# Kernel optimization log

Measured on AMD Instinct MI355X. Metric: run time of the kernel, lower is better.

Reference implementation:

```python
import jax, jax.numpy as jnp
import numpy as np
from jax import lax

H_SIZE = 2048
NUM_K = 16
NUM_V = 32
DK = 128
DV = 128
KDIM = NUM_K * DK      # 2048
VDIM = NUM_V * DV      # 4096
KCONV = 4
RMS_EPS = 1e-6
L2_EPS = 1e-6


def l2norm(x, eps=L2_EPS):
    # matches torch l2norm: x * rsqrt(sum(x^2, -1) + eps)
    return x * lax.rsqrt(jnp.sum(x * x, axis=-1, keepdims=True) + eps)


def setup_inputs() -> dict:
    key = jax.random.key(0)
    ks = jax.random.split(key, 7)
    B, S = 2, 1024
    conv_dim = 2 * KDIM + VDIM  # 8192
    return {
        "hidden_states": jax.random.normal(ks[0], (B, S, H_SIZE), jnp.float32),
        "w_qkvz": jax.random.normal(ks[1], (H_SIZE, 2 * KDIM + 2 * VDIM), jnp.float32) * 0.02,
        "w_ba": jax.random.normal(ks[2], (H_SIZE, 2 * NUM_V), jnp.float32) * 0.02,
        "conv_w": jax.random.normal(ks[3], (conv_dim, 1, KCONV), jnp.float32) * 0.2,  # depthwise [C,1,K]
        "dt_bias": jnp.ones((NUM_V,), jnp.float32),
        "A_log": jnp.log(jax.random.uniform(ks[4], (NUM_V,), jnp.float32, 0.5, 8.0)),
        "norm_w": jnp.ones((DV,), jnp.float32),
        "w_out": jax.random.normal(ks[5], (VDIM, H_SIZE), jnp.float32) * 0.02,
    }


def _forward(hidden_states, w_qkvz, w_ba, conv_w, dt_bias, A_log, norm_w, w_out):
    B, S, _ = hidden_states.shape
    rf = NUM_V // NUM_K  # GQA repeat factor = 2

    # input projections
    qkvz = hidden_states @ w_qkvz                                  # [B,S,12288]
    ba = hidden_states @ w_ba                                      # [B,S,64]

    # fix_query_key_value_ordering: group per k-head then split
    qkvz = qkvz.reshape(B, S, NUM_K, 2 * DK + 2 * rf * DV)
    q, k, v, z = jnp.split(qkvz, [DK, 2 * DK, 2 * DK + rf * DV], axis=3)
    ba = ba.reshape(B, S, NUM_K, 2 * rf)
    b, a = jnp.split(ba, [rf], axis=3)
    v = v.reshape(B, S, NUM_V, DV)
    z = z.reshape(B, S, NUM_V, DV)
    b = b.reshape(B, S, NUM_V)
    a = a.reshape(B, S, NUM_V)

    # depthwise causal conv over [q|k|v] channels + silu
    mixed = jnp.concatenate(
        [q.reshape(B, S, KDIM), k.reshape(B, S, KDIM), v.reshape(B, S, VDIM)], axis=-1
    )                                                              # [B,S,conv_dim]
    x = mixed.transpose(0, 2, 1)                                   # [B,C,S]
    x = jnp.pad(x, ((0, 0), (0, 0), (KCONV - 1, 0)))
    x = lax.conv_general_dilated(x, conv_w, window_strides=(1,), padding="VALID",
                                 feature_group_count=x.shape[1])
    x = jax.nn.silu(x).transpose(0, 2, 1)                          # [B,S,conv_dim]

    q, k, v = jnp.split(x, [KDIM, 2 * KDIM], axis=-1)
    q = q.reshape(B, S, NUM_K, DK)
    k = k.reshape(B, S, NUM_K, DK)
    v = v.reshape(B, S, NUM_V, DV)

    beta = jax.nn.sigmoid(b)                                       # [B,S,NUM_V]
    g = -jnp.exp(A_log) * jax.nn.softplus(a + dt_bias)             # log-decay [B,S,NUM_V]

    if rf > 1:
        q = jnp.repeat(q, rf, axis=2)                              # [B,S,NUM_V,DK]
        k = jnp.repeat(k, rf, axis=2)
    q = l2norm(q) * (DK ** -0.5)
    k = l2norm(k)

    # gated delta rule recurrence over time via lax.scan
    S0 = jnp.zeros((B, NUM_V, DK, DV), q.dtype)

    def step(state, inp):
        q_t, k_t, v_t, g_t, b_t = inp                              # [B,H,dk]/[B,H,dv]/[B,H]
        state = state * jnp.exp(g_t)[..., None, None]              # decay
        kv_mem = jnp.einsum("bhkv,bhk->bhv", state, k_t)
        delta = (v_t - kv_mem) * b_t[..., None]
        state = state + jnp.einsum("bhk,bhv->bhkv", k_t, delta)
        o = jnp.einsum("bhkv,bhk->bhv", state, q_t)
        return state, o

    xs = (jnp.moveaxis(q, 1, 0), jnp.moveaxis(k, 1, 0), jnp.moveaxis(v, 1, 0),
          jnp.moveaxis(g, 1, 0), jnp.moveaxis(beta, 1, 0))
    _, out = lax.scan(step, S0, xs)
    out = jnp.moveaxis(out, 0, 1)                                  # [B,S,NUM_V,DV]

    # gated RMSNorm (gate applied before normalization, Mamba2 style)
    xg = out * jax.nn.silu(z)
    y = xg * lax.rsqrt(jnp.mean(xg * xg, axis=-1, keepdims=True) + RMS_EPS) * norm_w
    y = y.reshape(B, S, VDIM)
    return y @ w_out                                               # [B,S,H_SIZE]


def reference(hidden_states, w_qkvz, w_ba, conv_w, dt_bias, A_log, norm_w, w_out):
    return _forward(hidden_states, w_qkvz, w_ba, conv_w, dt_bias, A_log, norm_w, w_out)
```

## Files before the change

kernel.cpp:

```cpp
#include <hip/hip_runtime.h>
#include <stdint.h>

#define AS1 __attribute__((address_space(1)))
#define AS3 __attribute__((address_space(3)))

typedef __bf16 bf16x8 __attribute__((ext_vector_type(8)));
typedef float f32x4 __attribute__((ext_vector_type(4)));

static __device__ __forceinline__ float bf2f(unsigned short u) {
    union { unsigned int i; float f; } x; x.i = ((unsigned int)u) << 16; return x.f;
}
static __device__ __forceinline__ unsigned short f2bf(float f) {
    union { float f; unsigned int i; } x; x.f = f;
    unsigned int u = x.i;
    unsigned int r = (u + 0x7fffu + ((u >> 16) & 1u)) >> 16;
    return (unsigned short)r;
}

static __device__ __forceinline__ void gll16(const void* g, void* l) {
    __builtin_amdgcn_global_load_lds((const AS1 unsigned int*)g,
                                     (AS3 unsigned int*)l, 16, 0, 0);
}

__global__ __launch_bounds__(256) void cvt_bf16_kernel(
    const float* __restrict__ src, unsigned short* __restrict__ dst, int n4) {
    int i = blockIdx.x * 256 + threadIdx.x;
    if (i >= n4) return;
    float4 v = ((const float4*)src)[i];
    ushort4 o;
    o.x = f2bf(v.x); o.y = f2bf(v.y); o.z = f2bf(v.z); o.w = f2bf(v.w);
    ((ushort4*)dst)[i] = o;
}

__global__ __launch_bounds__(256) void transpose_cvt_kernel(
    const float* __restrict__ src, unsigned short* __restrict__ dst, int R, int C) {
    __shared__ float tile[32][33];
    int x = threadIdx.x & 31, y = threadIdx.x >> 5;
    int c0 = blockIdx.x * 32, r0 = blockIdx.y * 32;
#pragma unroll
    for (int i = 0; i < 4; i++)
        tile[y + i * 8][x] = src[(size_t)(r0 + y + i * 8) * C + (c0 + x)];
    __syncthreads();
#pragma unroll
    for (int i = 0; i < 4; i++)
        dst[(size_t)(c0 + y + i * 8) * R + (r0 + x)] = f2bf(tile[x][y + i * 8]);
}

template <int MODE>
__global__ __launch_bounds__(512, 2) void gemm256_kernel(
    const unsigned short* __restrict__ A, const unsigned short* __restrict__ Bt,
    void* __restrict__ C, int M, int N, int K, int Ksl) {
    __shared__ __align__(16) unsigned short SH[65536];
    int tid = threadIdx.x;
    int lane = tid & 63, w = tid >> 6;
    int wr = w >> 2, wc = w & 3;
    int qd = lane >> 4, rc = lane & 15;

    int m0, n0, zz = 0;
    if (MODE == 0) {
        int wg = blockIdx.x;
        int xcd = wg & 7, loc = wg >> 3;
        m0 = (loc / 6) * 256;
        n0 = (xcd * 6 + loc % 6) * 256;
    } else {
        int wg = blockIdx.x;
        zz = wg >> 6;
        int loc = wg & 63;
        m0 = (loc >> 3) * 256;
        n0 = (loc & 7) * 256;
    }
    const int NT = Ksl >> 6;
    const int sK = K << 7;

    size_t sr[2];
#pragma unroll
    for (int j = 0; j < 2; j++) {
        int bu = j * 4096 + tid * 8;
        int sub = bu >> 9;
        int b = bu & 511;
        int bp = b ^ (((b >> 8) & 1) << 4);
        int row = ((sub >> 1) << 4) + (bp >> 5);
        int col = ((sub & 1) << 5) + (bp & 31);
        sr[j] = (size_t)row * K + col;
    }
    const unsigned short* Ab = A + (size_t)m0 * K + (size_t)zz * Ksl;
    const unsigned short* Bb = Bt + (size_t)n0 * K + (size_t)zz * Ksl;

    const int foff = (rc * 32 + qd * 8) ^ (((rc >> 3) & 1) << 4);
    const int Ah = wr;
    const int Bh = wc >> 1;
    const int brow4 = (wc & 1) * 4;

    f32x4 acc[8][4];
#pragma unroll
    for (int i = 0; i < 8; i++)
#pragma unroll
        for (int j = 0; j < 4; j++)
#pragma unroll
            for (int r = 0; r < 4; r++) acc[i][j][r] = 0.f;

    bf16x8 aq[4][2], bq[4][2];

#define STG(mat, h, t)                                                        \
    {                                                                         \
        const unsigned short* s_ = ((mat) ? Bb : Ab) + (h) * sK + (t) * 64;   \
        int d_ = ((mat) << 15) + (((((t) & 1) * 2 + (h))) << 13) + tid * 8;   \
        gll16(s_ + sr[0], &SH[d_]);                                           \
        gll16(s_ + sr[1], &SH[d_ + 4096]);                                    \
    }

#define LDAQ(p, QR)                                                           \
    {                                                                         \
        int ab_ = ((p) * 2 + Ah) * 8192 + (QR) * 4096 + foff;                 \
        _Pragma("unroll") for (int fi = 0; fi < 4; fi++)                      \
            _Pragma("unroll") for (int ks = 0; ks < 2; ks++)                  \
                aq[fi][ks] = *(const bf16x8*)&SH[ab_ + (fi * 2 + ks) * 512];  \
    }

#define LDBQ(p)                                                               \
    {                                                                         \
        int bb_ = 32768 + ((p) * 2 + Bh) * 8192 + brow4 * 1024 + foff;        \
        _Pragma("unroll") for (int fg = 0; fg < 4; fg++)                      \
            _Pragma("unroll") for (int ks = 0; ks < 2; ks++)                  \
                bq[fg][ks] = *(const bf16x8*)&SH[bb_ + (fg * 2 + ks) * 512];  \
    }

#define MFMAQ(QR, QC)                                                         \
    {                                                                         \
        _Pragma("unroll") for (int fi = 0; fi < 4; fi++)                      \
            _Pragma("unroll") for (int fj = 0; fj < 2; fj++)                  \
                _Pragma("unroll") for (int ks = 0; ks < 2; ks++)              \
                    acc[(QR) * 4 + fi][(QC) * 2 + fj] =                       \
                        __builtin_amdgcn_mfma_f32_16x16x32_bf16(              \
                            aq[fi][ks], bq[(QC) * 2 + fj][ks],                \
                            acc[(QR) * 4 + fi][(QC) * 2 + fj], 0, 0, 0);      \
    }

#define FENCE asm volatile("" ::: "memory")
#define BARRIER { FENCE; __builtin_amdgcn_s_barrier(); FENCE; }
#define LGKM0 asm volatile("s_waitcnt lgkmcnt(0)" ::: "memory")

    STG(0, 0, 0); STG(0, 1, 0); STG(1, 0, 0); STG(1, 1, 0);
    STG(1, 0, 1); STG(1, 1, 1); STG(0, 0, 1);
    asm volatile("s_waitcnt vmcnt(6)" ::: "memory");
    BARRIER;

    for (int g = 0; g < NT; ++g) {
        const int p = g & 1;
        LDAQ(p, 0);
        LDBQ(p);
        if (g + 1 < NT) STG(0, 1, g + 1);
        BARRIER; LGKM0;
        __builtin_amdgcn_s_setprio(1);
        MFMAQ(0, 0);
        __builtin_amdgcn_s_setprio(0);
        BARRIER;
        if (g + 2 < NT) STG(1, 0, g + 2);
        BARRIER; LGKM0;
        __builtin_amdgcn_s_setprio(1);
        MFMAQ(0, 1);
        __builtin_amdgcn_s_setprio(0);
        BARRIER;
        LDAQ(p, 1);
        if (g + 2 < NT) STG(1, 1, g + 2);
        BARRIER; LGKM0;
        __builtin_amdgcn_s_setprio(1);
        MFMAQ(1, 0);
        __builtin_amdgcn_s_setprio(0);
        BARRIER;
        if (g + 2 < NT) STG(0, 0, g + 2);
        if (g < NT - 2) { asm volatile("s_waitcnt vmcnt(6)" ::: "memory"); }
        else            { asm volatile("s_waitcnt vmcnt(0)" ::: "memory"); }
        BARRIER; LGKM0;
        __builtin_amdgcn_s_setprio(1);
        MFMAQ(1, 1);
        __builtin_amdgcn_s_setprio(0);
        BARRIER;
    }

#undef STG
#undef LDAQ
#undef LDBQ
#undef MFMAQ
#undef FENCE
#undef BARRIER
#undef LGKM0

    if (MODE == 0) {
        unsigned short* Cp = (unsigned short*)C;
#pragma unroll
        for (int mi = 0; mi < 8; mi++) {
            int row = m0 + wr * 128 + mi * 16 + qd * 4;
#pragma unroll
            for (int fg = 0; fg < 4; fg++) {
                int col = n0 + wc * 64 + fg * 16 + rc;
#pragma unroll
                for (int r = 0; r < 4; r++)
                    Cp[(size_t)(row + r) * N + col] = f2bf(acc[mi][fg][r]);
            }
        }
    } else {
        float* Cf = (float*)C + (size_t)zz * M * N;
#pragma unroll
        for (int mi = 0; mi < 8; mi++) {
            int row = m0 + wr * 128 + mi * 16 + qd * 4;
#pragma unroll
            for (int fg = 0; fg < 4; fg++) {
                int col = n0 + wc * 64 + fg * 16 + rc;
#pragma unroll
                for (int r = 0; r < 4; r++)
                    Cf[(size_t)(row + r) * N + col] = acc[mi][fg][r];
            }
        }
    }
}

__global__ __launch_bounds__(256) void add_out4_kernel(
    const float* __restrict__ p, float* __restrict__ out, int n4) {
    int i = blockIdx.x * 256 + threadIdx.x;
    if (i >= n4) return;
    size_t st = (size_t)n4 * 4;
    float4 a = ((const float4*)p)[i];
    float4 b = ((const float4*)(p + st))[i];
    float4 c = ((const float4*)(p + 2 * st))[i];
    float4 d = ((const float4*)(p + 3 * st))[i];
    ((float4*)out)[i] = make_float4(a.x + b.x + c.x + d.x, a.y + b.y + c.y + d.y,
                                    a.z + b.z + c.z + d.z, a.w + b.w + c.w + d.w);
}

__global__ __launch_bounds__(256) void bag_kernel(
    const float* __restrict__ hs, const float* __restrict__ w_ba,
    const float* __restrict__ A_log, const float* __restrict__ dt_bias,
    float* __restrict__ gg, float* __restrict__ bb) {
    int w = threadIdx.x >> 6, lane = threadIdx.x & 63;
    int r0 = blockIdx.x * 8 + w * 2;
    const float* h0 = hs + (size_t)r0 * 2048;
    float a0 = 0.f, a1 = 0.f;
    for (int k = 0; k < 2048; k++) {
        float wv = w_ba[k * 64 + lane];
        a0 += h0[k] * wv;
        a1 += h0[2048 + k] * wv;
    }
    int h = lane >> 2, idx = lane & 3;
    int vh = h * 2 + (idx & 1);
    float accs[2] = {a0, a1};
#pragma unroll
    for (int j = 0; j < 2; j++) {
        int t = r0 + j;
        float acc = accs[j];
        if (idx < 2) {
            bb[t * 32 + vh] = 1.f / (1.f + expf(-acc));
        } else {
            float x = acc + dt_bias[vh];
            float sp = fmaxf(x, 0.f) + log1pf(expf(-fabsf(x)));
            gg[t * 32 + vh] = -expf(A_log[vh]) * sp;
        }
    }
}

__global__ __launch_bounds__(256) void conv_kernel(
    const unsigned short* __restrict__ qkvz, const float* __restrict__ conv_w,
    unsigned short* __restrict__ qb, unsigned short* __restrict__ kb,
    float* __restrict__ vv) {
    __shared__ float xs[8192];
    __shared__ float rs[32];
    int t = blockIdx.x;
    int s = t & 1023;
    int tid = threadIdx.x;
    size_t rowbase = (size_t)t * 12288;
#pragma unroll
    for (int i = 0; i < 4; i++) {
        int c = (i * 256 + tid) * 8;
        int d = c & 127;
        int col;
        if (c < 2048) col = (c >> 7) * 768 + d;
        else if (c < 4096) col = ((c - 2048) >> 7) * 768 + 128 + d;
        else { int vh2 = (c - 4096) >> 7; col = (vh2 >> 1) * 768 + 256 + (vh2 & 1) * 128 + d; }
        float wts[8][4];
#pragma unroll
        for (int e = 0; e < 8; e++) {
            float4 t4 = *(const float4*)(conv_w + (size_t)(c + e) * 4);
            wts[e][0] = t4.x; wts[e][1] = t4.y; wts[e][2] = t4.z; wts[e][3] = t4.w;
        }
        float acc[8] = {0.f, 0.f, 0.f, 0.f, 0.f, 0.f, 0.f, 0.f};
#pragma unroll
        for (int j = 0; j < 4; j++) {
            int ss = s - 3 + j;
            if (ss >= 0) {
                uint4 u = *(const uint4*)(qkvz + rowbase + (size_t)(j - 3) * 12288 + col);
                const unsigned short* us = (const unsigned short*)&u;
#pragma unroll
                for (int e = 0; e < 8; e++) acc[e] += bf2f(us[e]) * wts[e][j];
            }
        }
#pragma unroll
        for (int e = 0; e < 8; e++) xs[c + e] = acc[e] / (1.f + expf(-acc[e]));
    }
    __syncthreads();
    {
        int seg = tid >> 3, part = tid & 7;
        const float* pp = xs + seg * 128 + part * 16;
        float s2 = 0.f;
#pragma unroll
        for (int j = 0; j < 16; j++) s2 += pp[j] * pp[j];
        s2 += __shfl_xor(s2, 1);
        s2 += __shfl_xor(s2, 2);
        s2 += __shfl_xor(s2, 4);
        if (part == 0) rs[seg] = rsqrtf(s2 + 1e-6f);
    }
    __syncthreads();
    const float QS = 0.08838834764831845f;
#pragma unroll
    for (int i = 0; i < 4; i++) {
        int c = (i * 256 + tid) * 8;
        float x[8];
#pragma unroll
        for (int e = 0; e < 8; e++) x[e] = xs[c + e];
        if (c < 4096) {
            float sc = (c < 2048) ? rs[c >> 7] * QS : rs[((c - 2048) >> 7) + 16];
            uint4 o;
            o.x = (unsigned)f2bf(x[0] * sc) | ((unsigned)f2bf(x[1] * sc) << 16);
            o.y = (unsigned)f2bf(x[2] * sc) | ((unsigned)f2bf(x[3] * sc) << 16);
            o.z = (unsigned)f2bf(x[4] * sc) | ((unsigned)f2bf(x[5] * sc) << 16);
            o.w = (unsigned)f2bf(x[6] * sc) | ((unsigned)f2bf(x[7] * sc) << 16);
            if (c < 2048) *(uint4*)(qb + (size_t)t * 2048 + c) = o;
            else *(uint4*)(kb + (size_t)t * 2048 + c - 2048) = o;
        } else {
            float* vp = vv + (size_t)t * 4096 + c - 4096;
            *(float4*)vp = make_float4(x[0], x[1], x[2], x[3]);
            *(float4*)(vp + 4) = make_float4(x[4], x[5], x[6], x[7]);
        }
    }
}

__global__ __launch_bounds__(256, 2) void prep_kernel(
    const unsigned short* __restrict__ qb, const unsigned short* __restrict__ kb,
    const float* __restrict__ vv, const float* __restrict__ gg,
    const float* __restrict__ bb,
    unsigned short* __restrict__ Wg, unsigned short* __restrict__ DlT,
    unsigned short* __restrict__ KtT, unsigned short* __restrict__ Pt,
    float* __restrict__ lamg, float* __restrict__ l64g) {
    __shared__ __align__(16) unsigned short Tb[64 * 72];
    __shared__ __align__(16) unsigned short Xw[4][64 * 72];
    __shared__ float Td[4 * 16 * 17];
    __shared__ float RHSw[4][16 * 68];
    __shared__ float cc[64], bet[64], lam_s[64], ex64[64];

    int bid = blockIdx.x;
    int ch = bid & 15, bh = bid >> 4;
    int vh = bh & 31, b = bh >> 5;
    int hk = vh >> 1;
    int t0 = b * 1024 + ch * 64;
    int tid = threadIdx.x, wv = tid >> 6, lane = tid & 63;
    int qd = lane >> 4, rc = lane & 15;
    int rowb = (wv & 1) * 32;
    size_t obase = (size_t)bid * 8192;
    size_t pbase = (size_t)bid * 4096;

    if (tid < 64) {
        float x = gg[(size_t)(t0 + tid) * 32 + vh];
#pragma unroll
        for (int ofs = 1; ofs < 64; ofs <<= 1) {
            float up = __shfl_up(x, ofs, 64);
            if (tid >= ofs) x += up;
        }
        cc[tid] = x;
        float l = __expf(x);
        lam_s[tid] = l;
        float tot = __shfl(x, 63, 64);
        ex64[tid] = __expf(tot - x);
        bet[tid] = bb[(size_t)(t0 + tid) * 32 + vh];
        lamg[(size_t)bid * 64 + tid] = l;
        if (tid == 0) l64g[bid] = __expf(tot);
    }
    __syncthreads();

    {
        const unsigned short* src = (wv >= 2) ? qb : kb;
        f32x4 acc[2][4];
#pragma unroll
        for (int tm = 0; tm < 2; tm++)
#pragma unroll
            for (int tn = 0; tn < 4; tn++)
#pragma unroll
                for (int r = 0; r < 4; r++) acc[tm][tn][r] = 0.f;
#pragma unroll
        for (int ks = 0; ks < 4; ks++) {
            bf16x8 af[2], bfr[4];
#pragma unroll
            for (int tm = 0; tm < 2; tm++) {
                int row = rowb + tm * 16 + rc;
                af[tm] = *(const bf16x8*)(src + ((size_t)(t0 + row) * 16 + hk) * 128 + ks * 32 + qd * 8);
            }
#pragma unroll
            for (int tn = 0; tn < 4; tn++)
                bfr[tn] = *(const bf16x8*)(kb + ((size_t)(t0 + tn * 16 + rc) * 16 + hk) * 128 + ks * 32 + qd * 8);
#pragma unroll
            for (int tm = 0; tm < 2; tm++)
#pragma unroll
                for (int tn = 0; tn < 4; tn++)
                    acc[tm][tn] = __builtin_amdgcn_mfma_f32_16x16x32_bf16(af[tm], bfr[tn], acc[tm][tn], 0, 0, 0);
        }
        if (wv < 2) {
#pragma unroll
            for (int tm = 0; tm < 2; tm++)
#pragma unroll
                for (int tn = 0; tn < 4; tn++)
#pragma unroll
                    for (int r = 0; r < 4; r++) {
                        int i = rowb + tm * 16 + qd * 4 + r;
                        int j = tn * 16 + rc;
                        float val = acc[tm][tn][r];
                        float tv = 0.f;
                        if (i > j) tv = bet[i] * __expf(cc[i] - cc[j]) * val;
                        Tb[i * 72 + j] = f2bf(-tv);
                        if ((i >> 4) == (j >> 4) && i > j)
                            Td[(i >> 4) * 272 + (i & 15) * 17 + (j & 15)] = tv;
                    }
        } else {
#pragma unroll
            for (int tm = 0; tm < 2; tm++)
#pragma unroll
                for (int tn = 0; tn < 4; tn++)
#pragma unroll
                    for (int r = 0; r < 4; r++) {
                        int i = rowb + tm * 16 + qd * 4 + r;
                        int j = tn * 16 + rc;
                        float ev = (i >= j) ? __expf(cc[i] - cc[j]) : 0.f;
                        Pt[pbase + i * 64 + j] = f2bf(ev * acc[tm][tn][r]);
                    }
        }
    }
    {
        int dk = tid >> 1, half = tid & 1;
#pragma unroll
        for (int j = 0; j < 4; j++) {
            unsigned short tmp[8];
#pragma unroll
            for (int e = 0; e < 8; e++) {
                int tok = half * 32 + j * 8 + e;
                tmp[e] = f2bf(bf2f(kb[((size_t)(t0 + tok) * 16 + hk) * 128 + dk]) * ex64[tok]);
            }
            *(uint4*)(KtT + obase + dk * 64 + half * 32 + j * 8) = *(const uint4*)tmp;
        }
    }
    __syncthreads();

    {
        int cb = wv;
        unsigned short* Xb = Xw[wv];
        float* RHS = RHSw[wv];
        for (int z = lane; z < 64 * 72 / 2; z += 64) ((unsigned int*)Xb)[z] = 0u;
#pragma unroll
        for (int B = 0; B < 4; B++) {
            f32x4 tacc[4];
#pragma unroll
            for (int cf = 0; cf < 4; cf++)
#pragma unroll
                for (int r = 0; r < 4; r++) {
                    int i = B * 16 + qd * 4 + r;
                    int c = cf * 16 + rc;
                    float v;
                    if (cb < 2)
                        v = bet[i] * vv[((size_t)(t0 + i) * 32 + vh) * 128 + cb * 64 + c];
                    else
                        v = bet[i] * lam_s[i] * bf2f(kb[((size_t)(t0 + i) * 16 + hk) * 128 + (cb - 2) * 64 + c]);
                    tacc[cf][r] = v;
                }
            __builtin_amdgcn_s_waitcnt(0xc07f);
            const int nks = (B + 1) >> 1;
#pragma unroll
            for (int ks = 0; ks < 2; ks++) {
                if (ks >= nks) break;
                bf16x8 af = *(const bf16x8*)&Tb[(B * 16 + rc) * 72 + ks * 32 + qd * 8];
#pragma unroll
                for (int cf = 0; cf < 4; cf++) {
                    bf16x8 bf_ = *(const bf16x8*)&Xb[(cf * 16 + rc) * 72 + ks * 32 + qd * 8];
                    tacc[cf] = __builtin_amdgcn_mfma_f32_16x16x32_bf16(af, bf_, tacc[cf], 0, 0, 0);
                }
            }
#pragma unroll
            for (int cf = 0; cf < 4; cf++)
#pragma unroll
                for (int r = 0; r < 4; r++)
                    RHS[(qd * 4 + r) * 68 + cf * 16 + rc] = tacc[cf][r];
            __builtin_amdgcn_s_waitcnt(0xc07f);
            {
                float d[16];
#pragma unroll
                for (int i2 = 0; i2 < 16; i2++) d[i2] = RHS[i2 * 68 + lane];
#pragma unroll
                for (int i2 = 1; i2 < 16; i2++)
#pragma unroll
                    for (int j2 = 0; j2 < i2; j2++)
                        d[i2] -= Td[B * 272 + i2 * 17 + j2] * d[j2];
#pragma unroll
                for (int i2 = 0; i2 < 16; i2++)
                    Xb[lane * 72 + B * 16 + i2] = f2bf(d[i2]);
            }
        }
        __builtin_amdgcn_s_waitcnt(0xc07f);
        if (cb < 2) {
#pragma unroll
            for (int j = 0; j < 8; j++) {
                uint4 u = *(const uint4*)&Xb[lane * 72 + j * 8];
                *(uint4*)(DlT + obase + (size_t)(cb * 64 + lane) * 64 + j * 8) = u;
            }
        } else {
#pragma unroll
            for (int dq = 0; dq < 8; dq++) {
                unsigned short tmp[8];
#pragma unroll
                for (int e = 0; e < 8; e++)
                    tmp[e] = Xb[(dq * 8 + e) * 72 + lane];
                *(uint4*)(Wg + obase + (size_t)lane * 128 + (cb - 2) * 64 + dq * 8) = *(const uint4*)tmp;
            }
        }
    }
}

__global__ __launch_bounds__(256, 2) void recb_kernel(
    const unsigned short* __restrict__ qb, const float* __restrict__ lamg,
    const float* __restrict__ l64g, const unsigned short* __restrict__ Wg,
    const unsigned short* __restrict__ DlT, const unsigned short* __restrict__ KtT,
    const unsigned short* __restrict__ Pt, float* __restrict__ oo) {
    __shared__ __align__(16) unsigned short St[16 * 136];
    __shared__ __align__(16) unsigned short Dls[16 * 72];
    int bid = blockIdx.x;
    int slice = bid >> 6;
    int rest = bid & 63;
    int vh = rest & 31, b = rest >> 5;
    int bh = b * 32 + vh;
    int hk = vh >> 1, dvo = slice * 16, tb = b * 1024;
    int tid = threadIdx.x, wv = tid >> 6, lane = tid & 63;
    int qd = lane >> 4, rc = lane & 15;

    f32x4 sacc[2];
#pragma unroll
    for (int tm = 0; tm < 2; tm++)
#pragma unroll
        for (int r = 0; r < 4; r++) sacc[tm][r] = 0.f;
    for (int z = tid; z < 16 * 136 / 2; z += 256) ((unsigned int*)St)[z] = 0u;
    __syncthreads();

#pragma unroll 1
    for (int ch = 0; ch < 16; ch++) {
        int bhch = bh * 16 + ch;
        size_t obase = (size_t)bhch * 8192;
        size_t pbase = (size_t)bhch * 4096;
        int t0 = tb + ch * 64;
        if (tid < 128) {
            int row = tid >> 3, t8 = (tid & 7) * 8;
            uint4 u = *(const uint4*)(DlT + obase + (dvo + row) * 64 + t8);
            *(uint4*)&Dls[row * 72 + t8] = u;
        }
        __syncthreads();
        {
            f32x4 uacc;
#pragma unroll
            for (int r = 0; r < 4; r++) uacc[r] = 0.f;
#pragma unroll
            for (int ks = 0; ks < 4; ks++) {
                bf16x8 a_ = *(const bf16x8*)&St[rc * 136 + ks * 32 + qd * 8];
                bf16x8 b_ = *(const bf16x8*)(Wg + obase + (size_t)(wv * 16 + rc) * 128 + ks * 32 + qd * 8);
                uacc = __builtin_amdgcn_mfma_f32_16x16x32_bf16(a_, b_, uacc, 0, 0, 0);
            }
#pragma unroll
            for (int r = 0; r < 4; r++) {
                int idx = (qd * 4 + r) * 72 + wv * 16 + rc;
                Dls[idx] = f2bf(bf2f(Dls[idx]) - uacc[r]);
            }
        }
        __syncthreads();
        {
            f32x4 qacc;
#pragma unroll
            for (int r = 0; r < 4; r++) qacc[r] = 0.f;
#pragma unroll
            for (int ks = 0; ks < 4; ks++) {
                bf16x8 a_ = *(const bf16x8*)(qb + ((size_t)(t0 + wv * 16 + rc) * 16 + hk) * 128 + ks * 32 + qd * 8);
                bf16x8 b_ = *(const bf16x8*)&St[rc * 136 + ks * 32 + qd * 8];
                qacc = __builtin_amdgcn_mfma_f32_16x16x32_bf16(a_, b_, qacc, 0, 0, 0);
            }
            bf16x8 bd[2];
#pragma unroll
            for (int ks = 0; ks < 2; ks++)
                bd[ks] = *(const bf16x8*)&Dls[rc * 72 + ks * 32 + qd * 8];
            f32x4 oacc;
#pragma unroll
            for (int r = 0; r < 4; r++)
                oacc[r] = lamg[(size_t)bhch * 64 + wv * 16 + qd * 4 + r] * qacc[r];
#pragma unroll
            for (int ks = 0; ks < 2; ks++) {
                bf16x8 a_ = *(const bf16x8*)(Pt + pbase + (size_t)(wv * 16 + rc) * 64 + ks * 32 + qd * 8);
                oacc = __builtin_amdgcn_mfma_f32_16x16x32_bf16(a_, bd[ks], oacc, 0, 0, 0);
            }
#pragma unroll
            for (int r = 0; r < 4; r++)
                oo[((size_t)(t0 + wv * 16 + qd * 4 + r) * 32 + vh) * 128 + dvo + rc] = oacc[r];
            float l64 = l64g[bhch];
#pragma unroll
            for (int tm = 0; tm < 2; tm++) {
#pragma unroll
                for (int r = 0; r < 4; r++) sacc[tm][r] *= l64;
#pragma unroll
                for (int ks = 0; ks < 2; ks++) {
                    bf16x8 a_ = *(const bf16x8*)(KtT + obase + (size_t)(wv * 32 + tm * 16 + rc) * 64 + ks * 32 + qd * 8);
                    sacc[tm] = __builtin_amdgcn_mfma_f32_16x16x32_bf16(a_, bd[ks], sacc[tm], 0, 0, 0);
                }
            }
        }
        __syncthreads();
#pragma unroll
        for (int tm = 0; tm < 2; tm++)
#pragma unroll
            for (int r = 0; r < 4; r++)
                St[rc * 136 + wv * 32 + tm * 16 + qd * 4 + r] = f2bf(sacc[tm][r]);
        __syncthreads();
    }
}

__global__ __launch_bounds__(256) void norm_kernel(
    const float* __restrict__ oo, const unsigned short* __restrict__ qkvz,
    const float* __restrict__ norm_w, unsigned short* __restrict__ yb) {
    int w = threadIdx.x >> 6, lane = threadIdx.x & 63;
    int g = blockIdx.x * 4 + w;
    int t = g >> 5, vh = g & 31;
    size_t ob = (size_t)g * 128;
    size_t zb = (size_t)t * 12288 + (size_t)(vh >> 1) * 768 + 512 + (vh & 1) * 128;
    float x0 = oo[ob + lane], x1 = oo[ob + 64 + lane];
    float z0 = bf2f(qkvz[zb + lane]), z1 = bf2f(qkvz[zb + 64 + lane]);
    float xg0 = x0 * (z0 / (1.f + expf(-z0)));
    float xg1 = x1 * (z1 / (1.f + expf(-z1)));
    float s = xg0 * xg0 + xg1 * xg1;
    s += __shfl_xor(s, 1);
    s += __shfl_xor(s, 2);
    s += __shfl_xor(s, 4);
    s += __shfl_xor(s, 8);
    s += __shfl_xor(s, 16);
    s += __shfl_xor(s, 32);
    float r = rsqrtf(s * (1.f / 128.f) + 1e-6f);
    size_t y0 = (size_t)t * 4096 + (size_t)vh * 128;
    yb[y0 + lane] = f2bf(xg0 * r * norm_w[lane]);
    yb[y0 + 64 + lane] = f2bf(xg1 * r * norm_w[64 + lane]);
}

extern "C" void kernel_launch(void* const* d_in, const int* in_sizes, int n_in,
                              void* d_out, int out_size, void* d_ws, size_t ws_size,
                              hipStream_t stream) {
    const float* hs      = (const float*)d_in[0];
    const float* w_qkvz  = (const float*)d_in[1];
    const float* w_ba    = (const float*)d_in[2];
    const float* conv_w  = (const float*)d_in[3];
    const float* dt_bias = (const float*)d_in[4];
    const float* A_log   = (const float*)d_in[5];
    const float* norm_w  = (const float*)d_in[6];
    const float* w_out   = (const float*)d_in[7];
    float* out = (float*)d_out;
    (void)in_sizes; (void)n_in; (void)out_size; (void)ws_size;

    char* p = (char*)d_ws;
    auto alloc = [&](size_t b) { char* r = p; p += (b + 255) & ~(size_t)255; return r; };
    float* gg = (float*)alloc(2048ull * 32 * 4);
    float* bb = (float*)alloc(2048ull * 32 * 4);
    unsigned short* hsb  = (unsigned short*)alloc(2048ull * 2048 * 2);
    unsigned short* woT  = (unsigned short*)alloc(2048ull * 4096 * 2);
    unsigned short* wqT  = (unsigned short*)alloc(12288ull * 2048 * 2);
    unsigned short* qkvz = (unsigned short*)alloc(2048ull * 12288 * 2);
    unsigned short* qb16 = (unsigned short*)alloc(2048ull * 2048 * 2);
    unsigned short* kb16 = (unsigned short*)alloc(2048ull * 2048 * 2);
    float* vv = (float*)alloc(2048ull * 4096 * 4);
    float* oo = (float*)alloc(2048ull * 4096 * 4);
    unsigned short* yb = (unsigned short*)alloc(2048ull * 4096 * 2);
    unsigned short* Wg  = (unsigned short*)alloc(1024ull * 8192 * 2);
    unsigned short* DlT = (unsigned short*)alloc(1024ull * 8192 * 2);
    unsigned short* KtT = (unsigned short*)alloc(1024ull * 8192 * 2);
    unsigned short* Pt  = (unsigned short*)alloc(1024ull * 4096 * 2);
    float* lamg = (float*)alloc(1024ull * 64 * 4);
    float* l64g = (float*)alloc(1024ull * 4);
    float* gpart = (float*)wqT;

    cvt_bf16_kernel<<<4096, 256, 0, stream>>>(hs, hsb, 2048 * 2048 / 4);
    transpose_cvt_kernel<<<dim3(12288 / 32, 2048 / 32), 256, 0, stream>>>(w_qkvz, wqT, 2048, 12288);
    transpose_cvt_kernel<<<dim3(2048 / 32, 4096 / 32), 256, 0, stream>>>(w_out, woT, 4096, 2048);
    gemm256_kernel<0><<<384, 512, 0, stream>>>(hsb, wqT, qkvz, 2048, 12288, 2048, 2048);
    bag_kernel<<<256, 256, 0, stream>>>(hs, w_ba, A_log, dt_bias, gg, bb);
    conv_kernel<<<2048, 256, 0, stream>>>(qkvz, conv_w, qb16, kb16, vv);
    prep_kernel<<<1024, 256, 0, stream>>>(qb16, kb16, vv, gg, bb, Wg, DlT, KtT, Pt, lamg, l64g);
    recb_kernel<<<512, 256, 0, stream>>>(qb16, lamg, l64g, Wg, DlT, KtT, Pt, oo);
    norm_kernel<<<16384, 256, 0, stream>>>(oo, qkvz, norm_w, yb);
    gemm256_kernel<1><<<256, 512, 0, stream>>>(yb, woT, gpart, 2048, 2048, 4096, 1024);
    add_out4_kernel<<<4096, 256, 0, stream>>>(gpart, out, 2048 * 2048 / 4);
}
```

Baseline: 733.5 us.

## Use 128x384 tiles for QKVZ projection GEMM and remap conv block order

Adds a dedicated GEMM kernel for the input projection that uses 128x384 output tiles, giving 512 workgroups instead of 384 so they divide evenly across the GPU's compute units and XCDs. The old MODE template is split into this kernel plus a float-output split-K kernel for the output projection. The conv kernel's block index is also remapped so blocks are interleaved across XCDs. The aim is better load balance with no tail wave, at the cost of a smaller M tile with less A reuse and a different LDS layout for B.

```diff
diff --git a/kernel.cpp b/kernel.cpp
--- a/kernel.cpp
+++ b/kernel.cpp
@@ -46,29 +46,164 @@
         dst[(size_t)(c0 + y + i * 8) * R + (r0 + x)] = f2bf(tile[x][y + i * 8]);
 }
 
-template <int MODE>
-__global__ __launch_bounds__(512, 2) void gemm256_kernel(
+#define FENCE asm volatile("" ::: "memory")
+#define BARRIER { FENCE; __builtin_amdgcn_s_barrier(); FENCE; }
+#define LGKM0 asm volatile("s_waitcnt lgkmcnt(0)" ::: "memory")
+
+__global__ __launch_bounds__(512, 2) void gemm384_kernel(
     const unsigned short* __restrict__ A, const unsigned short* __restrict__ Bt,
-    void* __restrict__ C, int M, int N, int K, int Ksl) {
+    unsigned short* __restrict__ C, int M, int N, int K) {
     __shared__ __align__(16) unsigned short SH[65536];
     int tid = threadIdx.x;
     int lane = tid & 63, w = tid >> 6;
     int wr = w >> 2, wc = w & 3;
     int qd = lane >> 4, rc = lane & 15;
 
-    int m0, n0, zz = 0;
-    if (MODE == 0) {
-        int wg = blockIdx.x;
-        int xcd = wg & 7, loc = wg >> 3;
-        m0 = (loc / 6) * 256;
-        n0 = (xcd * 6 + loc % 6) * 256;
-    } else {
-        int wg = blockIdx.x;
-        zz = wg >> 6;
-        int loc = wg & 63;
-        m0 = (loc >> 3) * 256;
-        n0 = (loc & 7) * 256;
-    }
+    int wg = blockIdx.x;
+    int xcd = wg & 7, loc = wg >> 3;
+    int m0 = (loc & 15) * 128;
+    int n0 = (xcd * 4 + (loc >> 4)) * 384;
+
+    const int NT = K >> 6;
+    const int sK = K << 7;
+
+    size_t sr[2];
+#pragma unroll
+    for (int j = 0; j < 2; j++) {
+        int bu = j * 4096 + tid * 8;
+        int sub = bu >> 9;
+        int b = bu & 511;
+        int bp = b ^ (((b >> 8) & 1) << 4);
+        int row = ((sub >> 1) << 4) + (bp >> 5);
+        int col = ((sub & 1) << 5) + (bp & 31);
+        sr[j] = (size_t)row * K + col;
+    }
+    const unsigned short* Ab = A + (size_t)m0 * K;
+    const unsigned short* Bb = Bt + (size_t)n0 * K;
+
+    const int foff = (rc * 32 + qd * 8) ^ (((rc >> 3) & 1) << 4);
+    int bC[6];
+#pragma unroll
+    for (int fj = 0; fj < 6; fj++) {
+        int nb = wc * 96 + fj * 16;
+        bC[fj] = (1 + (nb >> 7)) * 16384 + ((nb & 127) >> 4) * 1024 + foff;
+    }
+
+    f32x4 acc[4][6];
+#pragma unroll
+    for (int i = 0; i < 4; i++)
+#pragma unroll
+        for (int j = 0; j < 6; j++)
+#pragma unroll
+            for (int r = 0; r < 4; r++) acc[i][j][r] = 0.f;
+
+    bf16x8 aq[2][2], bq[6][2];
+
+#define STG(u, t)                                                             \
+    {                                                                         \
+        const unsigned short* s_ =                                            \
+            ((u) == 0 ? Ab : Bb + (size_t)((u)-1) * sK) + (size_t)(t) * 64;   \
+        int d_ = (((u)*2 + ((t)&1)) << 13) + tid * 8;                         \
+        gll16(s_ + sr[0], &SH[d_]);                                           \
+        gll16(s_ + sr[1], &SH[d_ + 4096]);                                    \
+    }
+
+#define LDAQ(p, QR)                                                           \
+    {                                                                         \
+        _Pragma("unroll") for (int fi = 0; fi < 2; fi++)                      \
+            _Pragma("unroll") for (int ks = 0; ks < 2; ks++)                  \
+                aq[fi][ks] = *(const bf16x8*)&SH[(p)*8192 +                   \
+                    (wr * 4 + (QR)*2 + fi) * 1024 + ks * 512 + foff];         \
+    }
+
+#define LDBQ(p)                                                               \
+    {                                                                         \
+        _Pragma("unroll") for (int fj = 0; fj < 6; fj++)                      \
+            _Pragma("unroll") for (int ks = 0; ks < 2; ks++)                  \
+                bq[fj][ks] = *(const bf16x8*)&SH[bC[fj] + (p)*8192 + ks*512]; \
+    }
+
+#define MFMAQ(QR, QC)                                                         \
+    {                                                                         \
+        _Pragma("unroll") for (int fi = 0; fi < 2; fi++)                      \
+            _Pragma("unroll") for (int fj = 0; fj < 3; fj++)                  \
+                _Pragma("unroll") for (int ks = 0; ks < 2; ks++)              \
+                    acc[(QR)*2 + fi][(QC)*3 + fj] =                           \
+                        __builtin_amdgcn_mfma_f32_16x16x32_bf16(              \
+                            aq[fi][ks], bq[(QC)*3 + fj][ks],                  \
+                            acc[(QR)*2 + fi][(QC)*3 + fj], 0, 0, 0);          \
+    }
+
+    STG(0, 0); STG(1, 0); STG(2, 0); STG(3, 0);
+    STG(1, 1); STG(2, 1); STG(3, 1);
+    asm volatile("s_waitcnt vmcnt(6)" ::: "memory");
+    BARRIER;
+
+    for (int g = 0; g < NT; ++g) {
+        const int p = g & 1;
+        LDAQ(p, 0);
+        LDBQ(p);
+        if (g + 1 < NT) STG(0, g + 1);
+        BARRIER; LGKM0;
+        __builtin_amdgcn_s_setprio(1);
+        MFMAQ(0, 0);
+        __builtin_amdgcn_s_setprio(0);
+        BARRIER;
+        if (g + 2 < NT) STG(1, g + 2);
+        BARRIER; LGKM0;
+        __builtin_amdgcn_s_setprio(1);
+        MFMAQ(0, 1);
+        __builtin_amdgcn_s_setprio(0);
+        BARRIER;
+        LDAQ(p, 1);
+        if (g + 2 < NT) STG(2, g + 2);
+        BARRIER; LGKM0;
+        __builtin_amdgcn_s_setprio(1);
+        MFMAQ(1, 0);
+        __builtin_amdgcn_s_setprio(0);
+        BARRIER;
+        if (g + 2 < NT) STG(3, g + 2);
+        if (g < NT - 2) { asm volatile("s_waitcnt vmcnt(6)" ::: "memory"); }
+        else            { asm volatile("s_waitcnt vmcnt(0)" ::: "memory"); }
+        BARRIER; LGKM0;
+        __builtin_amdgcn_s_setprio(1);
+        MFMAQ(1, 1);
+        __builtin_amdgcn_s_setprio(0);
+        BARRIER;
+    }
+
+#undef STG
+#undef LDAQ
+#undef LDBQ
+#undef MFMAQ
+
+#pragma unroll
+    for (int mi = 0; mi < 4; mi++) {
+        int row = m0 + wr * 64 + mi * 16 + qd * 4;
+#pragma unroll
+        for (int fj = 0; fj < 6; fj++) {
+            int col = n0 + wc * 96 + fj * 16 + rc;
+#pragma unroll
+            for (int r = 0; r < 4; r++)
+                C[(size_t)(row + r) * N + col] = f2bf(acc[mi][fj][r]);
+        }
+    }
+}
+
+__global__ __launch_bounds__(512, 2) void gemm256_kernel(
+    const unsigned short* __restrict__ A, const unsigned short* __restrict__ Bt,
+    float* __restrict__ C, int M, int N, int K, int Ksl) {
+    __shared__ __align__(16) unsigned short SH[65536];
+    int tid = threadIdx.x;
+    int lane = tid & 63, w = tid >> 6;
+    int wr = w >> 2, wc = w & 3;
+    int qd = lane >> 4, rc = lane & 15;
+
+    int wg = blockIdx.x;
+    int zz = wg >> 6;
+    int loc = wg & 63;
+    int m0 = (loc >> 3) * 256;
+    int n0 = (loc & 7) * 256;
     const int NT = Ksl >> 6;
     const int sK = K << 7;
 
@@ -135,10 +270,6 @@
                             aq[fi][ks], bq[(QC) * 2 + fj][ks],                \
                             acc[(QR) * 4 + fi][(QC) * 2 + fj], 0, 0, 0);      \
     }
-
-#define FENCE asm volatile("" ::: "memory")
-#define BARRIER { FENCE; __builtin_amdgcn_s_barrier(); FENCE; }
-#define LGKM0 asm volatile("s_waitcnt lgkmcnt(0)" ::: "memory")
 
     STG(0, 0, 0); STG(0, 1, 0); STG(1, 0, 0); STG(1, 1, 0);
     STG(1, 0, 1); STG(1, 1, 1); STG(0, 0, 1);
@@ -182,35 +313,17 @@
 #undef LDAQ
 #undef LDBQ
 #undef MFMAQ
-#undef FENCE
-#undef BARRIER
-#undef LGKM0
-
-    if (MODE == 0) {
-        unsigned short* Cp = (unsigned short*)C;
-#pragma unroll
-        for (int mi = 0; mi < 8; mi++) {
-            int row = m0 + wr * 128 + mi * 16 + qd * 4;
-#pragma unroll
-            for (int fg = 0; fg < 4; fg++) {
-                int col = n0 + wc * 64 + fg * 16 + rc;
-#pragma unroll
-                for (int r = 0; r < 4; r++)
-                    Cp[(size_t)(row + r) * N + col] = f2bf(acc[mi][fg][r]);
-            }
-        }
-    } else {
-        float* Cf = (float*)C + (size_t)zz * M * N;
-#pragma unroll
-        for (int mi = 0; mi < 8; mi++) {
-            int row = m0 + wr * 128 + mi * 16 + qd * 4;
-#pragma unroll
-            for (int fg = 0; fg < 4; fg++) {
-                int col = n0 + wc * 64 + fg * 16 + rc;
-#pragma unroll
-                for (int r = 0; r < 4; r++)
-                    Cf[(size_t)(row + r) * N + col] = acc[mi][fg][r];
-            }
+
+    float* Cf = C + (size_t)zz * M * N;
+#pragma unroll
+    for (int mi = 0; mi < 8; mi++) {
+        int row = m0 + wr * 128 + mi * 16 + qd * 4;
+#pragma unroll
+        for (int fg = 0; fg < 4; fg++) {
+            int col = n0 + wc * 64 + fg * 16 + rc;
+#pragma unroll
+            for (int r = 0; r < 4; r++)
+                Cf[(size_t)(row + r) * N + col] = acc[mi][fg][r];
         }
     }
 }
@@ -264,7 +377,7 @@
     float* __restrict__ vv) {
     __shared__ float xs[8192];
     __shared__ float rs[32];
-    int t = blockIdx.x;
+    int t = ((blockIdx.x & 7) << 8) + (blockIdx.x >> 3);
     int s = t & 1023;
     int tid = threadIdx.x;
     size_t rowbase = (size_t)t * 12288;
@@ -683,12 +796,12 @@
     cvt_bf16_kernel<<<4096, 256, 0, stream>>>(hs, hsb, 2048 * 2048 / 4);
     transpose_cvt_kernel<<<dim3(12288 / 32, 2048 / 32), 256, 0, stream>>>(w_qkvz, wqT, 2048, 12288);
     transpose_cvt_kernel<<<dim3(2048 / 32, 4096 / 32), 256, 0, stream>>>(w_out, woT, 4096, 2048);
-    gemm256_kernel<0><<<384, 512, 0, stream>>>(hsb, wqT, qkvz, 2048, 12288, 2048, 2048);
+    gemm384_kernel<<<512, 512, 0, stream>>>(hsb, wqT, qkvz, 2048, 12288, 2048);
     bag_kernel<<<256, 256, 0, stream>>>(hs, w_ba, A_log, dt_bias, gg, bb);
     conv_kernel<<<2048, 256, 0, stream>>>(qkvz, conv_w, qb16, kb16, vv);
     prep_kernel<<<1024, 256, 0, stream>>>(qb16, kb16, vv, gg, bb, Wg, DlT, KtT, Pt, lamg, l64g);
     recb_kernel<<<512, 256, 0, stream>>>(qb16, lamg, l64g, Wg, DlT, KtT, Pt, oo);
     norm_kernel<<<16384, 256, 0, stream>>>(oo, qkvz, norm_w, yb);
-    gemm256_kernel<1><<<256, 512, 0, stream>>>(yb, woT, gpart, 2048, 2048, 4096, 1024);
+    gemm256_kernel<<<256, 512, 0, stream>>>(yb, woT, gpart, 2048, 2048, 4096, 1024);
     add_out4_kernel<<<4096, 256, 0, stream>>>(gpart, out, 2048 * 2048 / 4);
 }
```

Result: no change. 719.6 us (-1.9%).
